# Performance work log

Measured on AMD Instinct MI355X. Metric: run time of the kernel, lower is better.

Reference implementation:

```python
import jax, jax.numpy as jnp
import numpy as np

B, C, H, Wd = 4, 64, 64, 64
CP = C // 2


def setup_inputs() -> dict:
    key = jax.random.key(0)
    k1, k2, k3 = jax.random.split(key, 3)
    Fq_l = jax.random.normal(k1, (B, C, H, Wd), dtype=jnp.float32)
    Fp_l = jax.random.normal(k2, (B, C, H, Wd), dtype=jnp.float32)
    # 1x1 conv == linear over channel dim; weight [out_c, in_c]
    W = jax.random.normal(k3, (CP, C), dtype=jnp.float32) * (1.0 / np.sqrt(C))
    b = jnp.zeros((CP,), dtype=jnp.float32)
    return {"Fq_l": Fq_l, "Fp_l": Fp_l, "W": W, "b": b}


def reference(Fq_l, Fp_l, W, b):
    bsz, c, h, w = Fq_l.shape
    hw = h * w
    # shared 1x1 conv projection: [b, c, h, w] -> [b, c//2, hw]
    q = jnp.einsum('oc,bchw->bohw', W, Fq_l).reshape(bsz, -1, hw) + b[None, :, None]
    p = jnp.einsum('oc,bchw->bohw', W, Fp_l).reshape(bsz, -1, hw) + b[None, :, None]
    # similarity: [b, hw, hw]
    sim = jnp.einsum('bcn,bcm->bnm', q, p)
    attn = jax.nn.softmax(sim, axis=-1)
    # aligned: [b, hw, c] -> [b, c, h, w]
    v = Fp_l.reshape(bsz, c, hw)
    aligned = jnp.einsum('bnm,bcm->bnc', attn, v)
    return aligned.transpose(0, 2, 1).reshape(bsz, c, h, w)
```

## Files before the change

kernel.cpp:

```cpp
#include <hip/hip_runtime.h>

#define HW 4096

typedef _Float16 half8  __attribute__((ext_vector_type(8)));
typedef __bf16   bf16x8 __attribute__((ext_vector_type(8)));
typedef float    f32x16 __attribute__((ext_vector_type(16)));

static __device__ __forceinline__ float fexp(float x) {
    return __expf(x);
}

static __device__ __forceinline__ unsigned cvtpk_bf16(float lo, float hi) {
    unsigned r;
    asm("v_cvt_pk_bf16_f32 %0, %1, %2" : "=v"(r) : "v"(lo), "v"(hi));
    return r;
}

static __device__ __forceinline__ f32x16 mfma16(uint4 a, uint4 b, f32x16 c) {
    return __builtin_amdgcn_mfma_f32_32x32x16_f16(
        __builtin_bit_cast(half8, a), __builtin_bit_cast(half8, b), c, 0, 0, 0);
}
static __device__ __forceinline__ f32x16 mfmab16(uint4 a, uint4 b, f32x16 c) {
    return __builtin_amdgcn_mfma_f32_32x32x16_bf16(
        __builtin_bit_cast(bf16x8, a), __builtin_bit_cast(bf16x8, b), c, 0, 0, 0);
}

__global__ __launch_bounds__(256) void prep_kernel(
    const float* __restrict__ Fq, const float* __restrict__ Fp,
    const float* __restrict__ W,  const float* __restrict__ bias,
    _Float16* __restrict__ q_ws, char* __restrict__ p_arr, char* __restrict__ v_arr)
{
    const int tid = threadIdx.x;
    const int b   = blockIdx.y;
    const int x   = blockIdx.x;

    if (x >= 64) {
        int mt = x - 64;
        int c5 = tid & 31, hi = (tid >> 5) & 1, chunk = (tid >> 6) & 1, chalf = tid >> 7;
        int c = chalf * 32 + c5;
        int m = mt * 32 + chunk * 16 + hi * 4;
        const float* src = Fp + ((size_t)(b * 64 + c) << 12) + m;
        float4 f0 = *(const float4*)src;
        float4 f1 = *(const float4*)(src + 8);
        uint4 o = make_uint4(cvtpk_bf16(f0.x, f0.y), cvtpk_bf16(f0.z, f0.w),
                             cvtpk_bf16(f1.x, f1.y), cvtpk_bf16(f1.z, f1.w));
        size_t tb = ((size_t)(((b * 128 + mt) * 2 + chalf) * 2 + chunk)) << 10;
        *(uint4*)(v_arr + tb + (size_t)((hi << 5) | c5) * 16) = o;
        return;
    }

    __shared__ float Wt[64][36];
    __shared__ float comb[128][33];

    for (int i = tid; i < 2048; i += 256)
        Wt[i & 63][i >> 6] = W[i];
    __syncthreads();

    const int isP   = x >> 5;
    const int nl    = tid & 127;
    const int chalf = tid >> 7;
    const int n     = ((x & 31) << 7) + nl;
    const float* in = (isP ? Fp : Fq) + (size_t)(b * 64 + chalf * 32) * HW + n;

    float acc[32];
    #pragma unroll
    for (int o = 0; o < 32; ++o) acc[o] = 0.f;

    for (int c = 0; c < 32; ++c) {
        float f = in[(size_t)c * HW];
        const float* wr = &Wt[chalf * 32 + c][0];
        #pragma unroll
        for (int o = 0; o < 32; o += 4) {
            float4 w4 = *(const float4*)(wr + o);
            acc[o]   += w4.x * f; acc[o+1] += w4.y * f;
            acc[o+2] += w4.z * f; acc[o+3] += w4.w * f;
        }
    }

    if (chalf) {
        #pragma unroll
        for (int o = 0; o < 32; ++o) comb[nl][o] = acc[o];
    }
    __syncthreads();
    if (chalf) return;

    #pragma unroll
    for (int o = 0; o < 32; ++o) acc[o] += comb[nl][o] + bias[o];

    if (!isP) {
        _Float16* dst = q_ws + ((size_t)(b * HW + n) << 5);
        #pragma unroll
        for (int g = 0; g < 4; ++g) {
            union { _Float16 h[8]; uint4 u; } pk;
            #pragma unroll
            for (int j = 0; j < 8; ++j) pk.h[j] = (_Float16)acc[g * 8 + j];
            *(uint4*)(dst + g * 8) = pk.u;
        }
    } else {
        int kt = n >> 5, ln = n & 31;
        #pragma unroll
        for (int chunk = 0; chunk < 2; ++chunk) {
            #pragma unroll
            for (int h2 = 0; h2 < 2; ++h2) {
                union { _Float16 h[8]; uint4 u; } pk;
                #pragma unroll
                for (int j = 0; j < 8; ++j) pk.h[j] = (_Float16)acc[chunk * 16 + h2 * 8 + j];
                size_t off = (((size_t)((b * 128 + kt) * 2 + chunk)) << 9) + (size_t)((h2 << 5) + ln) * 8;
                *(uint4*)(p_arr + off * 2) = pk.u;
            }
        }
    }
}

#define SOFTPART(S, A0, A1, LA, LB) { \
    float e0=fexp(S[0]),  e1=fexp(S[1]),  e2=fexp(S[2]),  e3=fexp(S[3]); \
    float e4=fexp(S[4]),  e5=fexp(S[5]),  e6=fexp(S[6]),  e7=fexp(S[7]); \
    float e8=fexp(S[8]),  e9=fexp(S[9]),  e10=fexp(S[10]), e11=fexp(S[11]); \
    float e12=fexp(S[12]), e13=fexp(S[13]), e14=fexp(S[14]), e15=fexp(S[15]); \
    LA += ((e0+e1)+(e2+e3)) + ((e4+e5)+(e6+e7)); \
    LB += ((e8+e9)+(e10+e11)) + ((e12+e13)+(e14+e15)); \
    A0 = make_uint4(cvtpk_bf16(e0,e1),  cvtpk_bf16(e2,e3),  cvtpk_bf16(e4,e5),  cvtpk_bf16(e6,e7)); \
    A1 = make_uint4(cvtpk_bf16(e8,e9),  cvtpk_bf16(e10,e11), cvtpk_bf16(e12,e13), cvtpk_bf16(e14,e15)); \
}

#define TILE(P0,P1,V00,V01,V10,V11) { \
    f32x16 s0 = (f32x16)0.0f, s1 = (f32x16)0.0f; \
    s0 = mfma16(P0, q00, s0); s0 = mfma16(P1, q01, s0); \
    s1 = mfma16(P0, q10, s1); s1 = mfma16(P1, q11, s1); \
    uint4 A0, A1; \
    SOFTPART(s0, A0, A1, l0a, l0b) \
    o00 = mfmab16(A0, V00, o00); o00 = mfmab16(A1, V01, o00); \
    o01 = mfmab16(A0, V10, o01); o01 = mfmab16(A1, V11, o01); \
    SOFTPART(s1, A0, A1, l1a, l1b) \
    o10 = mfmab16(A0, V00, o10); o10 = mfmab16(A1, V01, o10); \
    o11 = mfmab16(A0, V10, o11); o11 = mfmab16(A1, V11, o11); \
}

__global__ __launch_bounds__(512, 2) void attn_kernel(
    const _Float16* __restrict__ q_ws, const char* __restrict__ p_arr,
    const char* __restrict__ v_arr, float* __restrict__ out)
{
    __shared__ float part[8][32][33];
    __shared__ float l_red[8][2][64];
    __shared__ float l_inv[64];

    const int tid  = threadIdx.x;
    const int lane = tid & 63;
    const int w    = tid >> 6;
    const int lo5  = lane & 31;
    const int hi   = lane >> 5;

    const int id   = blockIdx.x + (blockIdx.y << 6);
    const int b    = (id >> 1) & 3;
    const int qb   = (((id >> 3) << 1) | (id & 1)) << 6;

    uint4 q00, q01, q10, q11;
    {
        const _Float16* qp = q_ws + (((size_t)(b * HW) + qb + lo5) << 5) + (hi << 3);
        q00 = *(const uint4*)qp;
        q01 = *(const uint4*)(qp + 16);
        q10 = *(const uint4*)(qp + 1024);
        q11 = *(const uint4*)(qp + 1040);
    }

    const char* pb = p_arr + ((size_t)(b * 128 + w * 16) << 11) + (lane << 4);
    const char* vb = v_arr + ((size_t)(b * 128 + w * 16) << 12) + (lane << 4);

    f32x16 o00 = (f32x16)0.0f, o01 = (f32x16)0.0f, o10 = (f32x16)0.0f, o11 = (f32x16)0.0f;
    float l0a = 0.f, l0b = 0.f, l1a = 0.f, l1b = 0.f;

    uint4 pA0, pA1, vA00, vA01, vA10, vA11;
    uint4 pB0, pB1, vB00, vB01, vB10, vB11;

#define LOADT(P0,P1,V00,V01,V10,V11,T) { \
    const char* pp = pb + ((size_t)(T) << 11); \
    P0 = *(const uint4*)pp; P1 = *(const uint4*)(pp + 1024); \
    const char* vp = vb + ((size_t)(T) << 12); \
    V00 = *(const uint4*)vp;          V01 = *(const uint4*)(vp + 1024); \
    V10 = *(const uint4*)(vp + 2048); V11 = *(const uint4*)(vp + 3072); }

    LOADT(pA0, pA1, vA00, vA01, vA10, vA11, 0)
    for (int i = 0; i < 8; ++i) {
        int t = 2 * i + 1;
        LOADT(pB0, pB1, vB00, vB01, vB10, vB11, t)
        TILE(pA0, pA1, vA00, vA01, vA10, vA11)
        int t2 = (t + 1 > 15) ? 15 : (t + 1);
        LOADT(pA0, pA1, vA00, vA01, vA10, vA11, t2)
        TILE(pB0, pB1, vB00, vB01, vB10, vB11)
    }

    l_red[w][0][lane] = l0a + l0b;
    l_red[w][1][lane] = l1a + l1b;
    __syncthreads();
    if (tid < 64) {
        int s_ = tid >> 5, qq = tid & 31;
        float sum = 0.f;
        #pragma unroll
        for (int w2 = 0; w2 < 8; ++w2)
            sum += l_red[w2][s_][qq] + l_red[w2][s_][qq + 32];
        l_inv[tid] = 1.0f / sum;
    }

#define EPIPASS(OC, S_, H_) { \
    __syncthreads(); \
    _Pragma("unroll") \
    for (int r = 0; r < 16; ++r) \
        part[w][(r & 3) + 8 * (r >> 2) + 4 * hi][lo5] = OC[r]; \
    __syncthreads(); \
    _Pragma("unroll") \
    for (int rep = 0; rep < 2; ++rep) { \
        int idx = rep * 512 + tid; \
        int c_ = idx >> 5, q_ = idx & 31; \
        float v_ = ((part[0][q_][c_] + part[1][q_][c_]) + (part[2][q_][c_] + part[3][q_][c_])) \
                 + ((part[4][q_][c_] + part[5][q_][c_]) + (part[6][q_][c_] + part[7][q_][c_])); \
        out[((size_t)(((b << 6) + ((H_) << 5) + c_)) << 12) + qb + ((S_) << 5) + q_] = v_ * l_inv[((S_) << 5) + q_]; \
    } \
}

    EPIPASS(o00, 0, 0)
    EPIPASS(o01, 0, 1)
    EPIPASS(o10, 1, 0)
    EPIPASS(o11, 1, 1)
}

extern "C" void kernel_launch(void* const* d_in, const int* in_sizes, int n_in,
                              void* d_out, int out_size, void* d_ws, size_t ws_size,
                              hipStream_t stream)
{
    const float* Fq = (const float*)d_in[0];
    const float* Fp = (const float*)d_in[1];
    const float* W  = (const float*)d_in[2];
    const float* bs = (const float*)d_in[3];
    float* out = (float*)d_out;

    _Float16* q_ws = (_Float16*)d_ws;
    char* p_arr = (char*)d_ws + (1 << 20);
    char* v_arr = (char*)d_ws + (2 << 20);

    prep_kernel<<<dim3(192, 4), 256, 0, stream>>>(Fq, Fp, W, bs, q_ws, p_arr, v_arr);
    attn_kernel<<<dim3(64, 4), 512, 0, stream>>>(q_ws, p_arr, v_arr, out);
}
```

Baseline: 30.73 us.

## Fold log2e into Q, use native exp2, packed sums, and MFMA priority

Scales the Q projection by log2(e) when it is stored, so the softmax can use the native exp2 instruction instead of __expf and its extra multiply. The row sums are accumulated with two-wide float vectors, which can map to packed adds. Both score tiles' exponentials are now computed before the PV MFMAs, and s_setprio is raised around that MFMA block so the matrix unit is issued ahead of the other wave's work. The cost is more live registers from holding both A/B fragments at once, plus a small rounding change because Q is scaled before the fp16 conversion.

```diff
diff --git a/kernel.cpp b/kernel.cpp
--- a/kernel.cpp
+++ b/kernel.cpp
@@ -1,13 +1,16 @@
 #include <hip/hip_runtime.h>
 
 #define HW 4096
+#define LOG2E 1.44269504088896340736f
 
 typedef _Float16 half8  __attribute__((ext_vector_type(8)));
 typedef __bf16   bf16x8 __attribute__((ext_vector_type(8)));
 typedef float    f32x16 __attribute__((ext_vector_type(16)));
-
-static __device__ __forceinline__ float fexp(float x) {
-    return __expf(x);
+typedef float    f32x2  __attribute__((ext_vector_type(2)));
+
+extern "C" __device__ float __ocml_native_exp2_f32(float);
+static __device__ __forceinline__ float fexp2(float x) {
+    return __ocml_native_exp2_f32(x);
 }
 
 static __device__ __forceinline__ unsigned cvtpk_bf16(float lo, float hi) {
@@ -93,7 +96,7 @@
         for (int g = 0; g < 4; ++g) {
             union { _Float16 h[8]; uint4 u; } pk;
             #pragma unroll
-            for (int j = 0; j < 8; ++j) pk.h[j] = (_Float16)acc[g * 8 + j];
+            for (int j = 0; j < 8; ++j) pk.h[j] = (_Float16)(acc[g * 8 + j] * LOG2E);
             *(uint4*)(dst + g * 8) = pk.u;
         }
     } else {
@@ -112,13 +115,16 @@
     }
 }
 
-#define SOFTPART(S, A0, A1, LA, LB) { \
-    float e0=fexp(S[0]),  e1=fexp(S[1]),  e2=fexp(S[2]),  e3=fexp(S[3]); \
-    float e4=fexp(S[4]),  e5=fexp(S[5]),  e6=fexp(S[6]),  e7=fexp(S[7]); \
-    float e8=fexp(S[8]),  e9=fexp(S[9]),  e10=fexp(S[10]), e11=fexp(S[11]); \
-    float e12=fexp(S[12]), e13=fexp(S[13]), e14=fexp(S[14]), e15=fexp(S[15]); \
-    LA += ((e0+e1)+(e2+e3)) + ((e4+e5)+(e6+e7)); \
-    LB += ((e8+e9)+(e10+e11)) + ((e12+e13)+(e14+e15)); \
+#define SOFTPART(S, A0, A1, LV) { \
+    float e0=fexp2(S[0]),  e1=fexp2(S[1]),  e2=fexp2(S[2]),  e3=fexp2(S[3]); \
+    float e4=fexp2(S[4]),  e5=fexp2(S[5]),  e6=fexp2(S[6]),  e7=fexp2(S[7]); \
+    float e8=fexp2(S[8]),  e9=fexp2(S[9]),  e10=fexp2(S[10]), e11=fexp2(S[11]); \
+    float e12=fexp2(S[12]), e13=fexp2(S[13]), e14=fexp2(S[14]), e15=fexp2(S[15]); \
+    f32x2 t0 = (f32x2){e0,e1}   + (f32x2){e2,e3}; \
+    f32x2 t1 = (f32x2){e4,e5}   + (f32x2){e6,e7}; \
+    f32x2 t2 = (f32x2){e8,e9}   + (f32x2){e10,e11}; \
+    f32x2 t3 = (f32x2){e12,e13} + (f32x2){e14,e15}; \
+    LV += (t0 + t1) + (t2 + t3); \
     A0 = make_uint4(cvtpk_bf16(e0,e1),  cvtpk_bf16(e2,e3),  cvtpk_bf16(e4,e5),  cvtpk_bf16(e6,e7)); \
     A1 = make_uint4(cvtpk_bf16(e8,e9),  cvtpk_bf16(e10,e11), cvtpk_bf16(e12,e13), cvtpk_bf16(e14,e15)); \
 }
@@ -127,13 +133,15 @@
     f32x16 s0 = (f32x16)0.0f, s1 = (f32x16)0.0f; \
     s0 = mfma16(P0, q00, s0); s0 = mfma16(P1, q01, s0); \
     s1 = mfma16(P0, q10, s1); s1 = mfma16(P1, q11, s1); \
-    uint4 A0, A1; \
-    SOFTPART(s0, A0, A1, l0a, l0b) \
+    uint4 A0, A1, B0, B1; \
+    SOFTPART(s0, A0, A1, l0v) \
+    SOFTPART(s1, B0, B1, l1v) \
+    __builtin_amdgcn_s_setprio(1); \
     o00 = mfmab16(A0, V00, o00); o00 = mfmab16(A1, V01, o00); \
     o01 = mfmab16(A0, V10, o01); o01 = mfmab16(A1, V11, o01); \
-    SOFTPART(s1, A0, A1, l1a, l1b) \
-    o10 = mfmab16(A0, V00, o10); o10 = mfmab16(A1, V01, o10); \
-    o11 = mfmab16(A0, V10, o11); o11 = mfmab16(A1, V11, o11); \
+    o10 = mfmab16(B0, V00, o10); o10 = mfmab16(B1, V01, o10); \
+    o11 = mfmab16(B0, V10, o11); o11 = mfmab16(B1, V11, o11); \
+    __builtin_amdgcn_s_setprio(0); \
 }
 
 __global__ __launch_bounds__(512, 2) void attn_kernel(
@@ -167,7 +175,7 @@
     const char* vb = v_arr + ((size_t)(b * 128 + w * 16) << 12) + (lane << 4);
 
     f32x16 o00 = (f32x16)0.0f, o01 = (f32x16)0.0f, o10 = (f32x16)0.0f, o11 = (f32x16)0.0f;
-    float l0a = 0.f, l0b = 0.f, l1a = 0.f, l1b = 0.f;
+    f32x2 l0v = (f32x2){0.f, 0.f}, l1v = (f32x2){0.f, 0.f};
 
     uint4 pA0, pA1, vA00, vA01, vA10, vA11;
     uint4 pB0, pB1, vB00, vB01, vB10, vB11;
@@ -189,8 +197,8 @@
         TILE(pB0, pB1, vB00, vB01, vB10, vB11)
     }
 
-    l_red[w][0][lane] = l0a + l0b;
-    l_red[w][1][lane] = l1a + l1b;
+    l_red[w][0][lane] = l0v.x + l0v.y;
+    l_red[w][1][lane] = l1v.x + l1v.y;
     __syncthreads();
     if (tid < 64) {
         int s_ = tid >> 5, qq = tid & 31;
```

Result: no change. 30.22 us (-1.7%).
